# Kernel optimization log

Measured on AMD Instinct MI355X. Metric: run time of the kernel, lower is better.

Reference implementation:

```python
import jax, jax.numpy as jnp
import numpy as np
from jax import lax

K = 5  # carafe kernel size


def conv2d(x, w, b=None, padding='SAME'):
    y = lax.conv_general_dilated(x, w, (1, 1), padding,
                                 dimension_numbers=('NHWC', 'HWIO', 'NHWC'))
    return y if b is None else y + b


def upsample2x(x):
    return jnp.repeat(jnp.repeat(x, 2, axis=1), 2, axis=2)


def carafe(coarse, kernel):
    # coarse: [B,H,W,C]; kernel: [B,2H,2W,K*K] predicted at fine resolution
    B, H, W, C = coarse.shape
    pad = K // 2
    p = jnp.pad(coarse, ((0, 0), (pad, pad), (pad, pad), (0, 0)))
    # [B,H,W,K*K,C] neighborhoods, row-major (di,dj) order
    patches = jnp.stack([p[:, di:di + H, dj:dj + W, :]
                         for di in range(K) for dj in range(K)], axis=3)
    # softmax-normalized reassembly weights; fine pixel (i,j) -> coarse (i//2,j//2)
    mask = jax.nn.softmax(kernel, axis=-1).reshape(B, H, 2, W, 2, K * K)
    out = jnp.einsum('bhxwyk,bhwkc->bhxwyc', mask, patches)
    return out.reshape(B, 2 * H, 2 * W, C)


def setup_inputs() -> dict:
    key = jax.random.key(0)
    ks = jax.random.split(key, 8)
    B, H, W = 4, 64, 64
    Cf, Cc, E, F = 128, 256, 64, 256
    s = lambda k, shape: jax.random.normal(k, shape, jnp.float32) * 0.05
    z = lambda n: jnp.zeros((n,), jnp.float32)
    return dict(
        fine=jax.random.normal(ks[0], (B, 2 * H, 2 * W, Cf), jnp.float32),
        coarse=jax.random.normal(ks[1], (B, H, W, Cc), jnp.float32),
        gate_w=s(ks[2], (1, 1, Cc, 1)), gate_b=z(1),
        ss_fine_w=s(ks[3], (1, 1, Cf, E)), ss_fine_b=z(E),
        ss_coarse_w=s(ks[4], (1, 1, Cc, E)),
        ss_content_w=s(ks[5], (3, 3, E, K * K)), ss_content_b=z(K * K),
        coarse_proj_w=s(ks[6], (1, 1, Cc, F)), coarse_proj_b=z(F),
        fine_proj_w=s(ks[7], (1, 1, F, F)), fine_proj_b=z(F),
    )


def reference(fine, coarse, gate_w, gate_b, ss_fine_w, ss_fine_b, ss_coarse_w,
              ss_content_w, ss_content_b, coarse_proj_w, coarse_proj_b,
              fine_proj_w, fine_proj_b):
    # gate branch: 1x1 conv + sigmoid on coarse, nearest-upsample to fine size
    gate = upsample2x(jax.nn.sigmoid(conv2d(coarse, gate_w, gate_b)))
    # SemiShift kernel prediction: shared 3x3 'content' conv on both embeddings
    f = conv2d(conv2d(fine, ss_fine_w, ss_fine_b), ss_content_w, ss_content_b)
    c = conv2d(conv2d(coarse, ss_coarse_w), ss_content_w, ss_content_b)
    kernel = f + upsample2x(c)  # [B,2H,2W,K*K]
    # CARAFE content-aware reassembly of coarse at fine resolution
    cu = carafe(coarse, kernel)
    c_out = conv2d(cu, coarse_proj_w, coarse_proj_b)
    # NOTE: faithful to source -- 'fine' projection is applied to the coarse output
    f_out = conv2d(c_out, fine_proj_w, fine_proj_b)
    return gate * f_out + (1.0 - gate) * c_out
```

## Files before the change

### kernel.cpp

```cpp
#include <hip/hip_runtime.h>
#include <math.h>

constexpr int Bb = 4, Hc = 64, Wc = 64, Cc = 256, Cf = 128, E = 64, KK = 25, F = 256;
constexpr int Hf = 128, Wf = 128;
constexpr int Nc = Bb * Hc * Wc;
constexpr int Nf = Bb * Hf * Wf;

typedef __attribute__((ext_vector_type(8))) short bf16x8;
typedef __attribute__((ext_vector_type(4))) float f32x4;

__device__ inline unsigned short f2b(float f) {
  union { float f; unsigned u; } v; v.f = f;
  return (unsigned short)((v.u + 0x7FFF + ((v.u >> 16) & 1)) >> 16);
}

__global__ __launch_bounds__(256) void prepA_kernel(
    const float* __restrict__ fw, const float* __restrict__ cw,
    const float* __restrict__ cntw, unsigned short* __restrict__ Wtf,
    unsigned short* __restrict__ Wtc, unsigned short* __restrict__ Wtcnt) {
  int gid = blockIdx.x * 256 + threadIdx.x;
  if (gid < 8192) {
    int i = gid;
    int n = i & 63, k = i >> 6;
    Wtf[n * 128 + k] = f2b(fw[i]);
  } else if (gid < 8192 + 16384) {
    int i = gid - 8192;
    int n = i & 63, k = i >> 6;
    Wtc[n * 256 + k] = f2b(cw[i]);
  } else if (gid < 8192 + 16384 + 18432) {
    int i = gid - 8192 - 16384;
    int n = i & 31, kk = i >> 5;
    Wtcnt[n * 576 + kk] = (n < 25) ? f2b(cntw[kk * 25 + n]) : (unsigned short)0;
  }
}

template <int K>
__device__ inline void emb_body(const float* __restrict__ in,
                                const unsigned short* __restrict__ Wt,
                                const float* __restrict__ bias,
                                unsigned short* __restrict__ out, int pxb,
                                unsigned short* a_s) {
  constexpr int LDA = K + 8;
  int t = threadIdx.x;
  constexpr int KC = K / 4;
  for (int idx = t; idx < 64 * KC; idx += 256) {
    int px = idx / KC, kc = idx % KC;
    float4 v = *(const float4*)&in[(size_t)(pxb + px) * K + kc * 4];
    *(short4*)&a_s[px * LDA + kc * 4] =
        make_short4((short)f2b(v.x), (short)f2b(v.y), (short)f2b(v.z), (short)f2b(v.w));
  }
  __syncthreads();

  int wid = t >> 6, lane = t & 63;
  int lr = lane & 15, lg = lane >> 4;
  const f32x4 zero4 = {0.f, 0.f, 0.f, 0.f};
  f32x4 acc[4] = {zero4, zero4, zero4, zero4};

  #pragma unroll
  for (int kt = 0; kt < K / 32; kt++) {
    bf16x8 a = *(const bf16x8*)&a_s[(wid * 16 + lr) * LDA + kt * 32 + lg * 8];
    #pragma unroll
    for (int nt = 0; nt < 4; nt++) {
      bf16x8 bb = *(const bf16x8*)&Wt[(size_t)(nt * 16 + lr) * K + kt * 32 + lg * 8];
      acc[nt] = __builtin_amdgcn_mfma_f32_16x16x32_bf16(a, bb, acc[nt], 0, 0, 0);
    }
  }

  #pragma unroll
  for (int nt = 0; nt < 4; nt++) {
    int n = nt * 16 + lr;
    float bv = bias ? bias[n] : 0.f;
    #pragma unroll
    for (int r = 0; r < 4; r++) {
      int px = wid * 16 + lg * 4 + r;
      out[(size_t)(pxb + px) * 64 + n] = f2b(acc[nt][r] + bv);
    }
  }
}

__global__ __launch_bounds__(256) void emb_prepB_kernel(
    const float* __restrict__ fine, const unsigned short* __restrict__ Wtf,
    const float* __restrict__ fbias, unsigned short* __restrict__ femb,
    const float* __restrict__ coarse, const unsigned short* __restrict__ Wtc,
    unsigned short* __restrict__ cemb,
    const float* __restrict__ W1, const float* __restrict__ W2,
    unsigned short* __restrict__ Wt1, unsigned short* __restrict__ Wt12,
    float* __restrict__ b12f, const float* __restrict__ b1,
    const float* __restrict__ b2, const float* __restrict__ gw,
    const float* __restrict__ gb, float* __restrict__ gatec) {
  __shared__ __align__(16) unsigned short pool[64 * 264];
  int idx = blockIdx.x, t = threadIdx.x;

  if (idx < Nf / 64) {
    emb_body<128>(fine, Wtf, fbias, femb, idx * 64, pool);
  } else if (idx < 1280) {
    emb_body<256>(coarse, Wtc, nullptr, cemb, (idx - Nf / 64) * 64, pool);
  } else if (idx < 1296) {
    float (*tile)[65] = (float(*)[65])pool;
    int sub = idx - 1280;
    int k0 = ((sub >> 2) & 3) * 64, n0 = (sub & 3) * 64;
    int r0 = t >> 6, c = t & 63;
    #pragma unroll
    for (int r = r0; r < 64; r += 4)
      tile[r][c] = W1[(size_t)(k0 + r) * 256 + n0 + c];
    __syncthreads();
    #pragma unroll
    for (int r = r0; r < 64; r += 4)
      Wt1[(size_t)(n0 + r) * 256 + k0 + c] = f2b(tile[c][r]);
  } else if (idx < 1312) {
    unsigned short* a_s = pool;
    unsigned short* b_s = pool + 64 * 72;
    int sub = idx - 1296;
    int nbase = (sub & 3) * 64, k0 = (sub >> 2) * 64;
    int wid = t >> 6, lane = t & 63;
    int lr = lane & 15, lg = lane >> 4;
    const f32x4 zero4 = {0.f, 0.f, 0.f, 0.f};
    f32x4 acc[4] = {zero4, zero4, zero4, zero4};

    for (int mc = 0; mc < 4; mc++) {
      for (int i = t; i < 64 * 16; i += 256) {
        int r = i >> 4, c4 = i & 15;
        float4 v = *(const float4*)&W1[(size_t)(k0 + r) * 256 + mc * 64 + c4 * 4];
        *(short4*)&a_s[r * 72 + c4 * 4] =
            make_short4((short)f2b(v.x), (short)f2b(v.y), (short)f2b(v.z), (short)f2b(v.w));
      }
      for (int i = t; i < 64 * 16; i += 256) {
        int m = i >> 4, n4 = i & 15;
        float4 v = *(const float4*)&W2[(size_t)(mc * 64 + m) * 256 + nbase + n4 * 4];
        b_s[(n4 * 4 + 0) * 72 + m] = f2b(v.x);
        b_s[(n4 * 4 + 1) * 72 + m] = f2b(v.y);
        b_s[(n4 * 4 + 2) * 72 + m] = f2b(v.z);
        b_s[(n4 * 4 + 3) * 72 + m] = f2b(v.w);
      }
      __syncthreads();
      #pragma unroll
      for (int kt = 0; kt < 2; kt++) {
        bf16x8 a = *(const bf16x8*)&a_s[(wid * 16 + lr) * 72 + kt * 32 + lg * 8];
        #pragma unroll
        for (int nt = 0; nt < 4; nt++) {
          bf16x8 bb = *(const bf16x8*)&b_s[(nt * 16 + lr) * 72 + kt * 32 + lg * 8];
          acc[nt] = __builtin_amdgcn_mfma_f32_16x16x32_bf16(a, bb, acc[nt], 0, 0, 0);
        }
      }
      __syncthreads();
    }
    #pragma unroll
    for (int nt = 0; nt < 4; nt++)
      #pragma unroll
      for (int r = 0; r < 4; r++)
        Wt12[(size_t)(nbase + nt * 16 + lr) * 256 + k0 + wid * 16 + lg * 4 + r] =
            f2b(acc[nt][r]);
  } else if (idx == 1312) {
    int n = t;
    float a0 = 0.f, a1 = 0.f, a2 = 0.f, a3 = 0.f;
    #pragma unroll 4
    for (int m = 0; m < 256; m += 4) {
      a0 += b1[m + 0] * W2[(size_t)(m + 0) * 256 + n];
      a1 += b1[m + 1] * W2[(size_t)(m + 1) * 256 + n];
      a2 += b1[m + 2] * W2[(size_t)(m + 2) * 256 + n];
      a3 += b1[m + 3] * W2[(size_t)(m + 3) * 256 + n];
    }
    b12f[n] = (a0 + a1) + (a2 + a3) + b2[n];
  } else {
    int w = t >> 6, lane = t & 63;
    int base = (idx - 1313) * 64 + w * 16;
    const float4 wv = *(const float4*)(gw + lane * 4);
    float gb0 = gb[0];
    #pragma unroll
    for (int rnd = 0; rnd < 2; rnd++) {
      int p0 = base + rnd * 8;
      float a0, a1, a2, a3, a4, a5, a6, a7;
      {
        float4 v0 = *(const float4*)(coarse + (size_t)(p0 + 0) * 256 + lane * 4);
        float4 v1 = *(const float4*)(coarse + (size_t)(p0 + 1) * 256 + lane * 4);
        float4 v2 = *(const float4*)(coarse + (size_t)(p0 + 2) * 256 + lane * 4);
        float4 v3 = *(const float4*)(coarse + (size_t)(p0 + 3) * 256 + lane * 4);
        float4 v4 = *(const float4*)(coarse + (size_t)(p0 + 4) * 256 + lane * 4);
        float4 v5 = *(const float4*)(coarse + (size_t)(p0 + 5) * 256 + lane * 4);
        float4 v6 = *(const float4*)(coarse + (size_t)(p0 + 6) * 256 + lane * 4);
        float4 v7 = *(const float4*)(coarse + (size_t)(p0 + 7) * 256 + lane * 4);
        a0 = v0.x * wv.x + v0.y * wv.y + v0.z * wv.z + v0.w * wv.w;
        a1 = v1.x * wv.x + v1.y * wv.y + v1.z * wv.z + v1.w * wv.w;
        a2 = v2.x * wv.x + v2.y * wv.y + v2.z * wv.z + v2.w * wv.w;
        a3 = v3.x * wv.x + v3.y * wv.y + v3.z * wv.z + v3.w * wv.w;
        a4 = v4.x * wv.x + v4.y * wv.y + v4.z * wv.z + v4.w * wv.w;
        a5 = v5.x * wv.x + v5.y * wv.y + v5.z * wv.z + v5.w * wv.w;
        a6 = v6.x * wv.x + v6.y * wv.y + v6.z * wv.z + v6.w * wv.w;
        a7 = v7.x * wv.x + v7.y * wv.y + v7.z * wv.z + v7.w * wv.w;
      }
      #pragma unroll
      for (int off2 = 32; off2; off2 >>= 1) {
        a0 += __shfl_xor(a0, off2);
        a1 += __shfl_xor(a1, off2);
        a2 += __shfl_xor(a2, off2);
        a3 += __shfl_xor(a3, off2);
        a4 += __shfl_xor(a4, off2);
        a5 += __shfl_xor(a5, off2);
        a6 += __shfl_xor(a6, off2);
        a7 += __shfl_xor(a7, off2);
      }
      if (lane == 0) {
        gatec[p0 + 0] = 1.f / (1.f + expf(-(a0 + gb0)));
        gatec[p0 + 1] = 1.f / (1.f + expf(-(a1 + gb0)));
        gatec[p0 + 2] = 1.f / (1.f + expf(-(a2 + gb0)));
        gatec[p0 + 3] = 1.f / (1.f + expf(-(a3 + gb0)));
        gatec[p0 + 4] = 1.f / (1.f + expf(-(a4 + gb0)));
        gatec[p0 + 5] = 1.f / (1.f + expf(-(a5 + gb0)));
        gatec[p0 + 6] = 1.f / (1.f + expf(-(a6 + gb0)));
        gatec[p0 + 7] = 1.f / (1.f + expf(-(a7 + gb0)));
      }
    }
  }
}

__global__ __launch_bounds__(256) void content_both_kernel(
    const unsigned short* __restrict__ femb, const unsigned short* __restrict__ cemb,
    const unsigned short* __restrict__ Wtcnt, const float* __restrict__ cb,
    float* __restrict__ kff, float* __restrict__ kfc) {
  __shared__ __align__(16) unsigned short a_s[324 * 72];
  int idx = blockIdx.x, t = threadIdx.x;
  const unsigned short* emb;
  float* out;
  int b, i0, j0, Hd, Wd;
  if (idx < 256) {
    b = idx >> 6; int rem = idx & 63;
    i0 = (rem >> 3) * 16; j0 = (rem & 7) * 16; Hd = 128; Wd = 128;
    emb = femb; out = kff;
  } else {
    int i2 = idx - 256;
    b = i2 >> 4; int rem = i2 & 15;
    i0 = (rem >> 2) * 16; j0 = (rem & 3) * 16; Hd = 64; Wd = 64;
    emb = cemb; out = kfc;
  }

  for (int i = t; i < 324 * 16; i += 256) {
    int cell = i >> 4, ck = i & 15;
    int gi = i0 - 1 + cell / 18;
    int gj = j0 - 1 + cell % 18;
    short4 v = make_short4(0, 0, 0, 0);
    if (gi >= 0 && gi < Hd && gj >= 0 && gj < Wd)
      v = *(const short4*)&emb[(size_t)((b * Hd + gi) * Wd + gj) * 64 + ck * 4];
    *(short4*)&a_s[cell * 72 + ck * 4] = v;
  }
  __syncthreads();

  int wid = t >> 6, lane = t & 63;
  int lr = lane & 15, lg = lane >> 4;
  const f32x4 zero4 = {0.f, 0.f, 0.f, 0.f};
  f32x4 acc[4][2];
  #pragma unroll
  for (int mt = 0; mt < 4; mt++)
    #pragma unroll
    for (int nt = 0; nt < 2; nt++) acc[mt][nt] = zero4;

  #pragma unroll
  for (int nt = 0; nt < 2; nt++) {
    bf16x8 wb[9][2];
    #pragma unroll
    for (int tap = 0; tap < 9; tap++)
      #pragma unroll
      for (int kt = 0; kt < 2; kt++)
        wb[tap][kt] = *(const bf16x8*)&Wtcnt[(size_t)(nt * 16 + lr) * 576 + tap * 64 + kt * 32 + lg * 8];

    #pragma unroll
    for (int mt = 0; mt < 4; mt++) {
      int m = wid * 4 + mt;
      #pragma unroll
      for (int di = 0; di < 3; di++) {
        #pragma unroll
        for (int dj = 0; dj < 3; dj++) {
          int cell = (m + di) * 18 + (lr + dj);
          int tap = di * 3 + dj;
          #pragma unroll
          for (int kt = 0; kt < 2; kt++) {
            bf16x8 a = *(const bf16x8*)&a_s[cell * 72 + kt * 32 + lg * 8];
            acc[mt][nt] = __builtin_amdgcn_mfma_f32_16x16x32_bf16(a, wb[tap][kt], acc[mt][nt], 0, 0, 0);
          }
        }
      }
    }
  }

  #pragma unroll
  for (int mt = 0; mt < 4; mt++) {
    int m = wid * 4 + mt;
    int gi = i0 + m;
    #pragma unroll
    for (int nt = 0; nt < 2; nt++) {
      int ch = nt * 16 + lr;
      if (ch < 25) {
        float bv = cb[ch];
        #pragma unroll
        for (int r = 0; r < 4; r++) {
          int gj = j0 + lg * 4 + r;
          out[(size_t)((b * Hd + gi) * Wd + gj) * 25 + ch] = acc[mt][nt][r] + bv;
        }
      }
    }
  }
}

__global__ __launch_bounds__(256) void carafe_kernel(
    const float* __restrict__ coarse, const float* __restrict__ kff,
    const float* __restrict__ kfc, unsigned short* __restrict__ cu_g) {
  __shared__ __align__(16) unsigned short buf[256 * 72];
  __shared__ __align__(16) unsigned short m_ext[64 * 72];
  unsigned short* win_t = buf;
  unsigned short* cu_s  = buf;

  int t = threadIdx.x;
  int b = blockIdx.z;
  int i0 = blockIdx.y * 8, j0 = blockIdx.x * 8;
  int hw0 = (i0 >> 1) - 2, ww0 = (j0 >> 1) - 2;

  {
    #pragma unroll
    for (int p0 = 0; p0 < 64; p0 += 4) {
      unsigned short vals[4];
      #pragma unroll
      for (int q = 0; q < 4; q++) {
        int p = p0 + q;
        int h = hw0 + (p >> 3), w = ww0 + (p & 7);
        float v = 0.f;
        if (h >= 0 && h < 64 && w >= 0 && w < 64)
          v = coarse[(size_t)((b * 64 + h) * 64 + w) * 256 + t];
        vals[q] = f2b(v);
      }
      *(short4*)&win_t[t * 72 + p0] =
          make_short4((short)vals[0], (short)vals[1], (short)vals[2], (short)vals[3]);
    }
  }
  if (t < 64) {
    int ti = t >> 3, tj = t & 7;
    int i = i0 + ti, j = j0 + tj;
    size_t fpx = (size_t)((b * 128 + i) * 128 + j);
    size_t cpx = (size_t)((b * 64 + (i >> 1)) * 64 + (j >> 1));
    float v[25];
    float mx = -1e30f;
    #pragma unroll
    for (int m = 0; m < 25; m++) {
      v[m] = kff[fpx * 25 + m] + kfc[cpx * 25 + m];
      mx = fmaxf(mx, v[m]);
    }
    float s = 0.f;
    #pragma unroll
    for (int m = 0; m < 25; m++) { v[m] = expf(v[m] - mx); s += v[m]; }
    float inv = 1.f / s;
    unsigned* row32 = (unsigned*)&m_ext[t * 72];
    #pragma unroll
    for (int q = 0; q < 36; q++) row32[q] = 0;
    int wib = ti >> 1, wjb = tj >> 1;
    #pragma unroll
    for (int di = 0; di < 5; di++)
      #pragma unroll
      for (int dj = 0; dj < 5; dj++)
        m_ext[t * 72 + (wib + di) * 8 + (wjb + dj)] = f2b(v[di * 5 + dj] * inv);
  }
  __syncthreads();

  int wid = t >> 6, lane = t & 63;
  int lr = lane & 15, lg = lane >> 4;
  const f32x4 zero4 = {0.f, 0.f, 0.f, 0.f};

  f32x4 acc0[4][4];
  #pragma unroll
  for (int mi = 0; mi < 4; mi++)
    #pragma unroll
    for (int ni = 0; ni < 4; ni++) acc0[mi][ni] = zero4;
  #pragma unroll
  for (int kt = 0; kt < 2; kt++) {
    bf16x8 am[4];
    #pragma unroll
    for (int mi = 0; mi < 4; mi++)
      am[mi] = *(const bf16x8*)&m_ext[(mi * 16 + lr) * 72 + kt * 32 + lg * 8];
    #pragma unroll
    for (int ni = 0; ni < 4; ni++) {
      bf16x8 bb = *(const bf16x8*)&win_t[(size_t)(wid * 64 + ni * 16 + lr) * 72 + kt * 32 + lg * 8];
      #pragma unroll
      for (int mi = 0; mi < 4; mi++)
        acc0[mi][ni] = __builtin_amdgcn_mfma_f32_16x16x32_bf16(am[mi], bb, acc0[mi][ni], 0, 0, 0);
    }
  }
  __syncthreads();

  #pragma unroll
  for (int mi = 0; mi < 4; mi++)
    #pragma unroll
    for (int ni = 0; ni < 4; ni++)
      #pragma unroll
      for (int r = 0; r < 4; r++)
        cu_s[(mi * 16 + lg * 4 + r) * 264 + wid * 64 + ni * 16 + lr] = f2b(acc0[mi][ni][r]);
  __syncthreads();

  for (int c = t; c < 2048; c += 256) {
    int p = c >> 5, off = (c & 31) << 3;
    int gi = i0 + (p >> 3), gj = j0 + (p & 7);
    bf16x8 v = *(const bf16x8*)&cu_s[p * 264 + off];
    *(bf16x8*)&cu_g[(size_t)((b * 128 + gi) * 128 + gj) * 256 + off] = v;
  }
}

__global__ __launch_bounds__(256, 2) void proj_kernel(
    const unsigned short* __restrict__ cu_g, const float* __restrict__ gatec,
    const unsigned short* __restrict__ Wt1, const float* __restrict__ b1,
    const unsigned short* __restrict__ Wt12, const float* __restrict__ b12,
    float* __restrict__ out) {
  __shared__ __align__(16) unsigned short a_s[2][64 * 264];
  __shared__ float g_s[2][32];
  int t = threadIdx.x;
  int bid = blockIdx.x;
  int cg = bid >> 8;
  int g  = bid & 255;
  int wid = t >> 6, lane = t & 63;
  int lr = lane & 15, lg = lane >> 4;
  int n0 = cg * 64 + wid * 16;

  bf16x8 wb1[8], wb12[8];
  #pragma unroll
  for (int kt = 0; kt < 8; kt++) {
    size_t wrow = (size_t)(n0 + lr) * 256 + kt * 32 + lg * 8;
    wb1[kt]  = *(const bf16x8*)&Wt1[wrow];
    wb12[kt] = *(const bf16x8*)&Wt12[wrow];
  }
  float b1v  = b1[n0 + lr];
  float b12v = b12[n0 + lr];

  {
    size_t m0 = (size_t)g * 256;
    for (int c = t; c < 2048; c += 256) {
      int row = c >> 5, off = (c & 31) << 3;
      *(bf16x8*)&a_s[0][row * 264 + off] = *(const bf16x8*)&cu_g[(m0 + row) * 256 + off];
    }
    if (t < 32) {
      int b_ = (int)(m0 >> 14), ii = (int)((m0 >> 7) & 127), j0 = (int)(m0 & 127);
      g_s[0][t] = gatec[(size_t)(b_ * 64 + (ii >> 1)) * 64 + (j0 >> 1) + t];
    }
  }
  __syncthreads();

  const f32x4 zero4 = {0.f, 0.f, 0.f, 0.f};

  for (int it = 0; it < 4; ++it) {
    int cur = it & 1, nxt = cur ^ 1;
    size_t m0i = (size_t)(g * 4 + it) * 64;

    bf16x8 pf[8];
    float gpf = 0.f;
    if (it < 3) {
      size_t m0n = m0i + 64;
      #pragma unroll
      for (int q = 0; q < 8; q++) {
        int c = t + q * 256;
        int row = c >> 5, off = (c & 31) << 3;
        pf[q] = *(const bf16x8*)&cu_g[(m0n + row) * 256 + off];
      }
      if (t < 32) {
        int b_ = (int)(m0n >> 14), ii = (int)((m0n >> 7) & 127), j0 = (int)(m0n & 127);
        gpf = gatec[(size_t)(b_ * 64 + (ii >> 1)) * 64 + (j0 >> 1) + t];
      }
    }

    f32x4 accc[4] = {zero4, zero4, zero4, zero4};
    f32x4 accf[4] = {zero4, zero4, zero4, zero4};
    #pragma unroll
    for (int kt = 0; kt < 8; kt++) {
      #pragma unroll
      for (int mi = 0; mi < 4; mi++) {
        bf16x8 a = *(const bf16x8*)&a_s[cur][(mi * 16 + lr) * 264 + kt * 32 + lg * 8];
        accc[mi] = __builtin_amdgcn_mfma_f32_16x16x32_bf16(a, wb1[kt],  accc[mi], 0, 0, 0);
        accf[mi] = __builtin_amdgcn_mfma_f32_16x16x32_bf16(a, wb12[kt], accf[mi], 0, 0, 0);
      }
    }

    if (it < 3) {
      #pragma unroll
      for (int q = 0; q < 8; q++) {
        int c = t + q * 256;
        int row = c >> 5, off = (c & 31) << 3;
        *(bf16x8*)&a_s[nxt][row * 264 + off] = pf[q];
      }
      if (t < 32) g_s[nxt][t] = gpf;
    }

    #pragma unroll
    for (int mi = 0; mi < 4; mi++) {
      #pragma unroll
      for (int r = 0; r < 4; r++) {
        int row = mi * 16 + lg * 4 + r;
        float gg = g_s[cur][row >> 1];
        float f_out = accf[mi][r] + b12v;
        float c_out = accc[mi][r] + b1v;
        out[(m0i + row) * 256 + n0 + lr] = gg * f_out + (1.f - gg) * c_out;
      }
    }

    if (it < 3) __syncthreads();
  }
}

extern "C" void kernel_launch(void* const* d_in, const int* in_sizes, int n_in,
                              void* d_out, int out_size, void* d_ws, size_t ws_size,
                              hipStream_t stream) {
  const float* fine        = (const float*)d_in[0];
  const float* coarse      = (const float*)d_in[1];
  const float* gate_w      = (const float*)d_in[2];
  const float* gate_b      = (const float*)d_in[3];
  const float* ss_fine_w   = (const float*)d_in[4];
  const float* ss_fine_b   = (const float*)d_in[5];
  const float* ss_coarse_w = (const float*)d_in[6];
  const float* ss_content_w= (const float*)d_in[7];
  const float* ss_content_b= (const float*)d_in[8];
  const float* W1          = (const float*)d_in[9];
  const float* b1          = (const float*)d_in[10];
  const float* W2          = (const float*)d_in[11];
  const float* b2          = (const float*)d_in[12];
  float* out = (float*)d_out;

  char* ws = (char*)d_ws;
  size_t off = 0;
  float* gatec = (float*)(ws + off); off += 131072;
  unsigned short* femb = (unsigned short*)(ws + off); off += (size_t)Nf * 64 * 2;
  unsigned short* cemb = (unsigned short*)(ws + off); off += (size_t)Nc * 64 * 2;
  float* kff   = (float*)(ws + off); off += (size_t)Nf * 25 * 4;
  float* kfc   = (float*)(ws + off); off += (size_t)Nc * 25 * 4;
  unsigned short* Wt1 = (unsigned short*)(ws + off); off += 65536 * 2;
  unsigned short* Wtf = (unsigned short*)(ws + off); off += 64 * 128 * 2;
  unsigned short* Wtc = (unsigned short*)(ws + off); off += 64 * 256 * 2;
  unsigned short* Wtcnt = (unsigned short*)(ws + off); off += 32 * 576 * 2;
  unsigned short* Wt12 = (unsigned short*)(ws + off); off += 65536 * 2;
  float* b12f = (float*)(ws + off); off += 1024;
  unsigned short* cu_g = (unsigned short*)(ws + off); off += (size_t)Nf * 256 * 2;

  prepA_kernel<<<168, 256, 0, stream>>>(ss_fine_w, ss_coarse_w, ss_content_w,
                                        Wtf, Wtc, Wtcnt);
  emb_prepB_kernel<<<1569, 256, 0, stream>>>(
      fine, Wtf, ss_fine_b, femb, coarse, Wtc, cemb,
      W1, W2, Wt1, Wt12, b12f, b1, b2, gate_w, gate_b, gatec);
  content_both_kernel<<<256 + 64, 256, 0, stream>>>(
      femb, cemb, Wtcnt, ss_content_b, kff, kfc);
  carafe_kernel<<<dim3(Wf / 8, Hf / 8, Bb), 256, 0, stream>>>(coarse, kff, kfc, cu_g);
  proj_kernel<<<1024, 256, 0, stream>>>(cu_g, gatec, Wt1, b1, Wt12, b12f, out);
}
```

Baseline: 114.1 us.

## Move gate and weight prep into content kernel, shrink embedding LDS tile

```diff
diff --git a/kernel.cpp b/kernel.cpp
--- a/kernel.cpp
+++ b/kernel.cpp
@@ -39,31 +39,33 @@
                                 const unsigned short* __restrict__ Wt,
                                 const float* __restrict__ bias,
                                 unsigned short* __restrict__ out, int pxb,
-                                unsigned short* a_s) {
-  constexpr int LDA = K + 8;
+                                unsigned short* a_s ) {
+  constexpr int LDA = 136;
   int t = threadIdx.x;
-  constexpr int KC = K / 4;
-  for (int idx = t; idx < 64 * KC; idx += 256) {
-    int px = idx / KC, kc = idx % KC;
-    float4 v = *(const float4*)&in[(size_t)(pxb + px) * K + kc * 4];
-    *(short4*)&a_s[px * LDA + kc * 4] =
-        make_short4((short)f2b(v.x), (short)f2b(v.y), (short)f2b(v.z), (short)f2b(v.w));
-  }
-  __syncthreads();
-
   int wid = t >> 6, lane = t & 63;
   int lr = lane & 15, lg = lane >> 4;
   const f32x4 zero4 = {0.f, 0.f, 0.f, 0.f};
   f32x4 acc[4] = {zero4, zero4, zero4, zero4};
 
   #pragma unroll
-  for (int kt = 0; kt < K / 32; kt++) {
-    bf16x8 a = *(const bf16x8*)&a_s[(wid * 16 + lr) * LDA + kt * 32 + lg * 8];
-    #pragma unroll
-    for (int nt = 0; nt < 4; nt++) {
-      bf16x8 bb = *(const bf16x8*)&Wt[(size_t)(nt * 16 + lr) * K + kt * 32 + lg * 8];
-      acc[nt] = __builtin_amdgcn_mfma_f32_16x16x32_bf16(a, bb, acc[nt], 0, 0, 0);
-    }
+  for (int c0 = 0; c0 < K; c0 += 128) {
+    for (int idx = t; idx < 64 * 32; idx += 256) {
+      int px = idx >> 5, kc = idx & 31;
+      float4 v = *(const float4*)&in[(size_t)(pxb + px) * K + c0 + kc * 4];
+      *(short4*)&a_s[px * LDA + kc * 4] =
+          make_short4((short)f2b(v.x), (short)f2b(v.y), (short)f2b(v.z), (short)f2b(v.w));
+    }
+    __syncthreads();
+    #pragma unroll
+    for (int kt = 0; kt < 4; kt++) {
+      bf16x8 a = *(const bf16x8*)&a_s[(wid * 16 + lr) * LDA + kt * 32 + lg * 8];
+      #pragma unroll
+      for (int nt = 0; nt < 4; nt++) {
+        bf16x8 bb = *(const bf16x8*)&Wt[(size_t)(nt * 16 + lr) * K + c0 + kt * 32 + lg * 8];
+        acc[nt] = __builtin_amdgcn_mfma_f32_16x16x32_bf16(a, bb, acc[nt], 0, 0, 0);
+      }
+    }
+    if (c0 + 128 < K) __syncthreads();
   }
 
   #pragma unroll
@@ -78,92 +80,33 @@
   }
 }
 
-__global__ __launch_bounds__(256) void emb_prepB_kernel(
+__global__ __launch_bounds__(256) void emb_both_kernel(
     const float* __restrict__ fine, const unsigned short* __restrict__ Wtf,
     const float* __restrict__ fbias, unsigned short* __restrict__ femb,
     const float* __restrict__ coarse, const unsigned short* __restrict__ Wtc,
-    unsigned short* __restrict__ cemb,
+    unsigned short* __restrict__ cemb) {
+  __shared__ __align__(16) unsigned short a_s[64 * 136];
+  int idx = blockIdx.x;
+  if (idx < Nf / 64) emb_body<128>(fine, Wtf, fbias, femb, idx * 64, a_s);
+  else               emb_body<256>(coarse, Wtc, nullptr, cemb, (idx - Nf / 64) * 64, a_s);
+}
+
+__global__ __launch_bounds__(256) void content_fused_kernel(
+    const unsigned short* __restrict__ femb, const unsigned short* __restrict__ cemb,
+    const unsigned short* __restrict__ Wtcnt, const float* __restrict__ cb,
+    float* __restrict__ kff, float* __restrict__ kfc,
+    const float* __restrict__ coarse, const float* __restrict__ gw,
+    const float* __restrict__ gb, float* __restrict__ gatec,
     const float* __restrict__ W1, const float* __restrict__ W2,
     unsigned short* __restrict__ Wt1, unsigned short* __restrict__ Wt12,
     float* __restrict__ b12f, const float* __restrict__ b1,
-    const float* __restrict__ b2, const float* __restrict__ gw,
-    const float* __restrict__ gb, float* __restrict__ gatec) {
-  __shared__ __align__(16) unsigned short pool[64 * 264];
+    const float* __restrict__ b2) {
+  __shared__ __align__(16) unsigned short a_s[324 * 72];
   int idx = blockIdx.x, t = threadIdx.x;
 
-  if (idx < Nf / 64) {
-    emb_body<128>(fine, Wtf, fbias, femb, idx * 64, pool);
-  } else if (idx < 1280) {
-    emb_body<256>(coarse, Wtc, nullptr, cemb, (idx - Nf / 64) * 64, pool);
-  } else if (idx < 1296) {
-    float (*tile)[65] = (float(*)[65])pool;
-    int sub = idx - 1280;
-    int k0 = ((sub >> 2) & 3) * 64, n0 = (sub & 3) * 64;
-    int r0 = t >> 6, c = t & 63;
-    #pragma unroll
-    for (int r = r0; r < 64; r += 4)
-      tile[r][c] = W1[(size_t)(k0 + r) * 256 + n0 + c];
-    __syncthreads();
-    #pragma unroll
-    for (int r = r0; r < 64; r += 4)
-      Wt1[(size_t)(n0 + r) * 256 + k0 + c] = f2b(tile[c][r]);
-  } else if (idx < 1312) {
-    unsigned short* a_s = pool;
-    unsigned short* b_s = pool + 64 * 72;
-    int sub = idx - 1296;
-    int nbase = (sub & 3) * 64, k0 = (sub >> 2) * 64;
-    int wid = t >> 6, lane = t & 63;
-    int lr = lane & 15, lg = lane >> 4;
-    const f32x4 zero4 = {0.f, 0.f, 0.f, 0.f};
-    f32x4 acc[4] = {zero4, zero4, zero4, zero4};
-
-    for (int mc = 0; mc < 4; mc++) {
-      for (int i = t; i < 64 * 16; i += 256) {
-        int r = i >> 4, c4 = i & 15;
-        float4 v = *(const float4*)&W1[(size_t)(k0 + r) * 256 + mc * 64 + c4 * 4];
-        *(short4*)&a_s[r * 72 + c4 * 4] =
-            make_short4((short)f2b(v.x), (short)f2b(v.y), (short)f2b(v.z), (short)f2b(v.w));
-      }
-      for (int i = t; i < 64 * 16; i += 256) {
-        int m = i >> 4, n4 = i & 15;
-        float4 v = *(const float4*)&W2[(size_t)(mc * 64 + m) * 256 + nbase + n4 * 4];
-        b_s[(n4 * 4 + 0) * 72 + m] = f2b(v.x);
-        b_s[(n4 * 4 + 1) * 72 + m] = f2b(v.y);
-        b_s[(n4 * 4 + 2) * 72 + m] = f2b(v.z);
-        b_s[(n4 * 4 + 3) * 72 + m] = f2b(v.w);
-      }
-      __syncthreads();
-      #pragma unroll
-      for (int kt = 0; kt < 2; kt++) {
-        bf16x8 a = *(const bf16x8*)&a_s[(wid * 16 + lr) * 72 + kt * 32 + lg * 8];
-        #pragma unroll
-        for (int nt = 0; nt < 4; nt++) {
-          bf16x8 bb = *(const bf16x8*)&b_s[(nt * 16 + lr) * 72 + kt * 32 + lg * 8];
-          acc[nt] = __builtin_amdgcn_mfma_f32_16x16x32_bf16(a, bb, acc[nt], 0, 0, 0);
-        }
-      }
-      __syncthreads();
-    }
-    #pragma unroll
-    for (int nt = 0; nt < 4; nt++)
-      #pragma unroll
-      for (int r = 0; r < 4; r++)
-        Wt12[(size_t)(nbase + nt * 16 + lr) * 256 + k0 + wid * 16 + lg * 4 + r] =
-            f2b(acc[nt][r]);
-  } else if (idx == 1312) {
-    int n = t;
-    float a0 = 0.f, a1 = 0.f, a2 = 0.f, a3 = 0.f;
-    #pragma unroll 4
-    for (int m = 0; m < 256; m += 4) {
-      a0 += b1[m + 0] * W2[(size_t)(m + 0) * 256 + n];
-      a1 += b1[m + 1] * W2[(size_t)(m + 1) * 256 + n];
-      a2 += b1[m + 2] * W2[(size_t)(m + 2) * 256 + n];
-      a3 += b1[m + 3] * W2[(size_t)(m + 3) * 256 + n];
-    }
-    b12f[n] = (a0 + a1) + (a2 + a3) + b2[n];
-  } else {
+  if (idx < 256) {
     int w = t >> 6, lane = t & 63;
-    int base = (idx - 1313) * 64 + w * 16;
+    int base = idx * 64 + w * 16;
     const float4 wv = *(const float4*)(gw + lane * 4);
     float gb0 = gb[0];
     #pragma unroll
@@ -210,24 +153,88 @@
         gatec[p0 + 7] = 1.f / (1.f + expf(-(a7 + gb0)));
       }
     }
-  }
-}
-
-__global__ __launch_bounds__(256) void content_both_kernel(
-    const unsigned short* __restrict__ femb, const unsigned short* __restrict__ cemb,
-    const unsigned short* __restrict__ Wtcnt, const float* __restrict__ cb,
-    float* __restrict__ kff, float* __restrict__ kfc) {
-  __shared__ __align__(16) unsigned short a_s[324 * 72];
-  int idx = blockIdx.x, t = threadIdx.x;
+    return;
+  } else if (idx < 272) {
+    float (*tile)[65] = (float(*)[65])a_s;
+    int sub = idx - 256;
+    int k0 = ((sub >> 2) & 3) * 64, n0 = (sub & 3) * 64;
+    int r0 = t >> 6, c = t & 63;
+    #pragma unroll
+    for (int r = r0; r < 64; r += 4)
+      tile[r][c] = W1[(size_t)(k0 + r) * 256 + n0 + c];
+    __syncthreads();
+    #pragma unroll
+    for (int r = r0; r < 64; r += 4)
+      Wt1[(size_t)(n0 + r) * 256 + k0 + c] = f2b(tile[c][r]);
+    return;
+  } else if (idx < 288) {
+    unsigned short* aa = a_s;
+    unsigned short* bs = a_s + 64 * 72;
+    int sub = idx - 272;
+    int nbase = (sub & 3) * 64, k0 = (sub >> 2) * 64;
+    int wid = t >> 6, lane = t & 63;
+    int lr = lane & 15, lg = lane >> 4;
+    const f32x4 zero4 = {0.f, 0.f, 0.f, 0.f};
+    f32x4 acc[4] = {zero4, zero4, zero4, zero4};
+
+    for (int mc = 0; mc < 4; mc++) {
+      for (int i = t; i < 64 * 16; i += 256) {
+        int r = i >> 4, c4 = i & 15;
+        float4 v = *(const float4*)&W1[(size_t)(k0 + r) * 256 + mc * 64 + c4 * 4];
+        *(short4*)&aa[r * 72 + c4 * 4] =
+            make_short4((short)f2b(v.x), (short)f2b(v.y), (short)f2b(v.z), (short)f2b(v.w));
+      }
+      for (int i = t; i < 64 * 16; i += 256) {
+        int m = i >> 4, n4 = i & 15;
+        float4 v = *(const float4*)&W2[(size_t)(mc * 64 + m) * 256 + nbase + n4 * 4];
+        bs[(n4 * 4 + 0) * 72 + m] = f2b(v.x);
+        bs[(n4 * 4 + 1) * 72 + m] = f2b(v.y);
+        bs[(n4 * 4 + 2) * 72 + m] = f2b(v.z);
+        bs[(n4 * 4 + 3) * 72 + m] = f2b(v.w);
+      }
+      __syncthreads();
+      #pragma unroll
+      for (int kt = 0; kt < 2; kt++) {
+        bf16x8 a = *(const bf16x8*)&aa[(wid * 16 + lr) * 72 + kt * 32 + lg * 8];
+        #pragma unroll
+        for (int nt = 0; nt < 4; nt++) {
+          bf16x8 bb = *(const bf16x8*)&bs[(nt * 16 + lr) * 72 + kt * 32 + lg * 8];
+          acc[nt] = __builtin_amdgcn_mfma_f32_16x16x32_bf16(a, bb, acc[nt], 0, 0, 0);
+        }
+      }
+      __syncthreads();
+    }
+    #pragma unroll
+    for (int nt = 0; nt < 4; nt++)
+      #pragma unroll
+      for (int r = 0; r < 4; r++)
+        Wt12[(size_t)(nbase + nt * 16 + lr) * 256 + k0 + wid * 16 + lg * 4 + r] =
+            f2b(acc[nt][r]);
+    return;
+  } else if (idx == 288) {
+    int n = t;
+    float a0 = 0.f, a1 = 0.f, a2 = 0.f, a3 = 0.f;
+    #pragma unroll 4
+    for (int m = 0; m < 256; m += 4) {
+      a0 += b1[m + 0] * W2[(size_t)(m + 0) * 256 + n];
+      a1 += b1[m + 1] * W2[(size_t)(m + 1) * 256 + n];
+      a2 += b1[m + 2] * W2[(size_t)(m + 2) * 256 + n];
+      a3 += b1[m + 3] * W2[(size_t)(m + 3) * 256 + n];
+    }
+    b12f[n] = (a0 + a1) + (a2 + a3) + b2[n];
+    return;
+  }
+
+  int cidx = idx - 289;
   const unsigned short* emb;
   float* out;
   int b, i0, j0, Hd, Wd;
-  if (idx < 256) {
-    b = idx >> 6; int rem = idx & 63;
+  if (cidx < 256) {
+    b = cidx >> 6; int rem = cidx & 63;
     i0 = (rem >> 3) * 16; j0 = (rem & 7) * 16; Hd = 128; Wd = 128;
     emb = femb; out = kff;
   } else {
-    int i2 = idx - 256;
+    int i2 = cidx - 256;
     b = i2 >> 4; int rem = i2 & 15;
     i0 = (rem >> 2) * 16; j0 = (rem & 3) * 16; Hd = 64; Wd = 64;
     emb = cemb; out = kfc;
@@ -533,11 +540,11 @@
 
   prepA_kernel<<<168, 256, 0, stream>>>(ss_fine_w, ss_coarse_w, ss_content_w,
                                         Wtf, Wtc, Wtcnt);
-  emb_prepB_kernel<<<1569, 256, 0, stream>>>(
-      fine, Wtf, ss_fine_b, femb, coarse, Wtc, cemb,
-      W1, W2, Wt1, Wt12, b12f, b1, b2, gate_w, gate_b, gatec);
-  content_both_kernel<<<256 + 64, 256, 0, stream>>>(
-      femb, cemb, Wtcnt, ss_content_b, kff, kfc);
+  emb_both_kernel<<<Nf / 64 + Nc / 64, 256, 0, stream>>>(
+      fine, Wtf, ss_fine_b, femb, coarse, Wtc, cemb);
+  content_fused_kernel<<<289 + 256 + 64, 256, 0, stream>>>(
+      femb, cemb, Wtcnt, ss_content_b, kff, kfc,
+      coarse, gate_w, gate_b, gatec, W1, W2, Wt1, Wt12, b12f, b1, b2);
   carafe_kernel<<<dim3(Wf / 8, Hf / 8, Bb), 256, 0, stream>>>(coarse, kff, kfc, cu_g);
   proj_kernel<<<1024, 256, 0, stream>>>(cu_g, gatec, Wt1, b1, Wt12, b12f, out);
 }
```

Measured after the change: 114.4 us. No clear change (+0.3%).
